# Kernel optimization log

Hardware: AMD Instinct MI355X
Metric: run time of the kernel (lower is better)

## Reference

```python
import jax, jax.numpy as jnp
import numpy as np

B, L, DM, DI, N = 8, 2048, 512, 768, 8  # batch, seq, d_model, d_inner=int(1.5*512), d_state


def setup_inputs() -> dict:
    key = jax.random.key(0)
    ks = jax.random.split(key, 8)
    g = lambda k, shape, sc=1.0: (jax.random.normal(k, shape, jnp.float32) * sc)
    return {
        "x": g(ks[0], (B, L, DM)),
        "W_in": g(ks[1], (DM, 2 * DI), 0.02),    # in_proj weight (stored in->out)
        "A_log": g(ks[2], (DI, N)),               # nn.Parameter(randn)
        "D_param": g(ks[3], (DI,)),               # skip-connection D
        "W_x": g(ks[4], (DI, N), 0.02),           # x_proj weight
        "W_dt": g(ks[5], (N, DI), 0.02),          # dt_proj weight
        "b_dt": jnp.zeros((DI,), jnp.float32),    # dt_proj bias
        "W_out": g(ks[6], (DI, DM), 0.02),        # out_proj weight
    }


def reference(x, W_in, A_log, D_param, W_x, W_dt, b_dt, W_out):
    xz = x @ W_in                                  # (B,L,2*DI)
    d_inner = W_in.shape[1] // 2
    x_ssm, z = xz[..., :d_inner], xz[..., d_inner:]
    x_ssm = jax.nn.silu(x_ssm)                     # (B,L,DI)
    A = -jnp.exp(A_log.astype(jnp.float32))        # (DI,N)
    delta = jax.nn.softplus((x_ssm @ W_x) @ W_dt + b_dt)  # (B,L,DI)

    n_state = A.shape[-1]

    def step(h, inp):
        xt, dt = inp                               # each (B,DI)
        dA = jnp.exp(dt[..., None] * A)            # (B,DI,N)
        h = dA * h + dt[..., None] * xt[..., None]
        y = jnp.sum(h, axis=-1) + D_param * xt     # (B,DI)
        return h, y

    h0 = jnp.zeros((x.shape[0], d_inner, n_state), x_ssm.dtype)
    xs = (jnp.swapaxes(x_ssm, 0, 1), jnp.swapaxes(delta, 0, 1))  # (L,B,DI)
    _, ys = jax.lax.scan(step, h0, xs)             # ys: (L,B,DI)
    y = jnp.swapaxes(ys, 0, 1)                     # (B,L,DI)
    y = y * jax.nn.silu(z)
    return y @ W_out                               # (B,L,DM)
```

## Files before the change

### kernel.cpp

```cpp
#include <hip/hip_runtime.h>

typedef unsigned short bfu;
typedef __attribute__((ext_vector_type(8))) short short8;
typedef __attribute__((ext_vector_type(4))) float f32x4;

__device__ __forceinline__ float bf2f(bfu u){
  union { unsigned int i; float f; } v; v.i = ((unsigned int)u) << 16; return v.f;
}
__device__ __forceinline__ bfu f2bf(float f){
  union { float f; unsigned int i; } v; v.f = f;
  unsigned int r = (v.i + 0x7FFFu + ((v.i >> 16) & 1u)) >> 16;
  return (bfu)r;
}
__device__ __forceinline__ float fexp2(float x){ return __builtin_amdgcn_exp2f(x); }
__device__ __forceinline__ float flog2(float x){ return __builtin_amdgcn_logf(x); }
__device__ __forceinline__ float softplusf(float x){
  float t = fexp2(-fabsf(x) * 1.44269504088896f);
  return fmaxf(x, 0.f) + 0.69314718055995f * flog2(1.f + t);
}
__device__ __forceinline__ void gload16(const bfu* g, bfu* l){
  __builtin_amdgcn_global_load_lds((const __attribute__((address_space(1))) unsigned int*)g,
                                   (__attribute__((address_space(3))) unsigned int*)l, 16, 0, 0);
}

__global__ __launch_bounds__(256) void cvt_all_kernel(const float* __restrict__ x, bfu* __restrict__ x_bf,
                                                      const float* __restrict__ W_in, const float* __restrict__ W_out,
                                                      const float* __restrict__ W_x,
                                                      bfu* __restrict__ WinT, bfu* __restrict__ WoutT,
                                                      float* __restrict__ WxT){
  int g = blockIdx.x * 256 + threadIdx.x;
  if (g < 2097152){
    float4 v = ((const float4*)x)[g];
    ushort4 o;
    o.x = f2bf(v.x); o.y = f2bf(v.y); o.z = f2bf(v.z); o.w = f2bf(v.w);
    ((ushort4*)x_bf)[g] = o;
    return;
  }
  int h = g - 2097152;
  if (h < 786432){
    int r = h % 512, c = h / 512;
    WinT[h] = f2bf(W_in[(size_t)r * 1536 + c]);
  } else if (h < 786432 + 393216){
    int h2 = h - 786432;
    int r = h2 % 768, c = h2 / 768;
    WoutT[h2] = f2bf(W_out[(size_t)r * 512 + c]);
  } else if (h < 786432 + 393216 + 6144){
    int h2 = h - (786432 + 393216);
    int n = h2 / 768, k = h2 % 768;
    WxT[h2] = W_x[(size_t)k * 8 + n];
  }
}

template<int EPI, int KK>
__global__ __launch_bounds__(256)
void gemm_db(const bfu* __restrict__ Amat, const bfu* __restrict__ Bt,
             void* __restrict__ out0, void* __restrict__ out1,
             int NBN, int N)
{
  constexpr int NT = KK / 64;
  __shared__ bfu As[2 * 128 * 64];
  __shared__ bfu Bs[2 * 128 * 64];
  const int tid  = threadIdx.x;
  const int lane = tid & 63;
  const int w    = tid >> 6;
  const int wr   = w >> 1, wc = w & 1;

  const int cpx = gridDim.x >> 3;
  const int id  = blockIdx.x;
  const int nid = (id & 7) * cpx + (id >> 3);
  const int bn  = nid % NBN;
  const int bm  = nid / NBN;

  const int srow = tid >> 3;
  const int scol = ((tid & 7) ^ (srow & 7)) * 8;
  const bfu* gA = Amat + ((size_t)(bm * 128 + srow)) * KK + scol;
  const bfu* gB = Bt   + ((size_t)(bn * 128 + srow)) * KK + scol;
  bfu* lA = As + tid * 8;
  bfu* lB = Bs + tid * 8;

  auto STAGE = [&](int t, int sel){
    const int k0 = t * 64;
    #pragma unroll
    for (int i = 0; i < 4; i++){
      gload16(gA + (size_t)(i * 32) * KK + k0, lA + sel * 8192 + i * 2048);
      gload16(gB + (size_t)(i * 32) * KK + k0, lB + sel * 8192 + i * 2048);
    }
  };

  f32x4 acc[4][4];
  #pragma unroll
  for (int i = 0; i < 4; i++)
    #pragma unroll
    for (int j = 0; j < 4; j++)
      #pragma unroll
      for (int r = 0; r < 4; r++) acc[i][j][r] = 0.f;

  STAGE(0, 0);
  STAGE(1, 1);

  #pragma unroll
  for (int t = 0; t < NT; ++t){
    if (t + 1 < NT) asm volatile("s_waitcnt vmcnt(8)" ::: "memory");
    else            asm volatile("s_waitcnt vmcnt(0)" ::: "memory");
    __builtin_amdgcn_s_barrier();

    const bfu* Ab = As + (t & 1) * 8192;
    const bfu* Bb = Bs + (t & 1) * 8192;
    #pragma unroll
    for (int kk = 0; kk < 2; kk++){
      short8 a[4], b[4];
      const int sA = ((kk * 4 + (lane >> 4)) ^ (lane & 7)) * 8;
      #pragma unroll
      for (int m = 0; m < 4; m++){
        int r = wr * 64 + m * 16 + (lane & 15);
        a[m] = *(const short8*)&Ab[r * 64 + sA];
      }
      #pragma unroll
      for (int n = 0; n < 4; n++){
        int r = wc * 64 + n * 16 + (lane & 15);
        b[n] = *(const short8*)&Bb[r * 64 + sA];
      }
      __builtin_amdgcn_s_setprio(1);
      #pragma unroll
      for (int m = 0; m < 4; m++)
        #pragma unroll
        for (int n = 0; n < 4; n++)
          acc[m][n] = __builtin_amdgcn_mfma_f32_16x16x32_bf16(a[m], b[n], acc[m][n], 0, 0, 0);
      __builtin_amdgcn_s_setprio(0);
    }
    __builtin_amdgcn_s_barrier();
    if (t + 2 < NT) STAGE(t + 2, t & 1);
  }

  #pragma unroll
  for (int m = 0; m < 4; m++){
    #pragma unroll
    for (int n = 0; n < 4; n++){
      const int row0 = bm * 128 + wr * 64 + m * 16 + (lane >> 4) * 4;
      const int col  = bn * 128 + wc * 64 + n * 16 + (lane & 15);
      #pragma unroll
      for (int r = 0; r < 4; r++){
        float v = acc[m][n][r];
        int row = row0 + r;
        if (EPI == 0){
          float s = v / (1.f + __expf(-v));
          if (col < 768) ((bfu*)out0)[(size_t)row * 768 + col]         = f2bf(s);
          else           ((bfu*)out1)[(size_t)row * 768 + (col - 768)] = f2bf(s);
        } else {
          ((float*)out0)[(size_t)row * N + col] = v;
        }
      }
    }
  }
}

__global__ __launch_bounds__(256) void u_kernel(const bfu* __restrict__ xssm, const float* __restrict__ WxT,
                                                float* __restrict__ u){
  int wid = threadIdx.x >> 6, lane = threadIdx.x & 63;
  int row = blockIdx.x * 4 + wid;
  const bfu* xr = xssm + (size_t)row * 768;
  float acc[8];
  #pragma unroll
  for (int n = 0; n < 8; n++) acc[n] = 0.f;
  #pragma unroll
  for (int i = 0; i < 3; i++){
    int kb = i * 256 + lane * 4;
    ushort4 xq = *(const ushort4*)(xr + kb);
    float x0 = bf2f(xq.x), x1 = bf2f(xq.y), x2 = bf2f(xq.z), x3 = bf2f(xq.w);
    #pragma unroll
    for (int n = 0; n < 8; n++){
      float4 wv = *(const float4*)(WxT + (size_t)n * 768 + kb);
      acc[n] += x0 * wv.x + x1 * wv.y + x2 * wv.z + x3 * wv.w;
    }
  }
  #pragma unroll
  for (int n = 0; n < 8; n++){
    #pragma unroll
    for (int off = 32; off >= 1; off >>= 1) acc[n] += __shfl_xor(acc[n], off, 64);
  }
  if (lane == 0){
    float4 o0 = { acc[0], acc[1], acc[2], acc[3] };
    float4 o1 = { acc[4], acc[5], acc[6], acc[7] };
    *(float4*)(u + (size_t)row * 8)     = o0;
    *(float4*)(u + (size_t)row * 8 + 4) = o1;
  }
}

__global__ __launch_bounds__(128) void scan_phase1(const bfu* __restrict__ xssm, const float* __restrict__ u,
    const float* __restrict__ Wdt, const float* __restrict__ bdt, const float* __restrict__ A_log,
    float* __restrict__ Pws, float* __restrict__ Hws){
  int tid = threadIdx.x;
  int bid = blockIdx.x;
  int b = bid / 192; int rem = bid % 192;
  int c = rem / 3;   int dblk = rem % 3;
  int d0 = dblk * 256 + tid * 2;
  float Al2[2][8], H[2][8], Wr[2][8], bd[2], S[2];
  #pragma unroll
  for (int j = 0; j < 2; j++){
    bd[j] = bdt[d0 + j];
    S[j] = 0.f;
    #pragma unroll
    for (int n = 0; n < 8; n++){
      Al2[j][n] = -__expf(A_log[(size_t)(d0 + j) * 8 + n]) * 1.4426950408889634f;
      Wr[j][n]  = Wdt[(size_t)n * 768 + d0 + j];
      H[j][n] = 0.f;
    }
  }
  int r0 = b * 2048 + c * 32;
  size_t base = (size_t)r0 * 768 + d0;
  #pragma unroll 8
  for (int i = 0; i < 32; i++){
    float4 u0 = *(const float4*)(u + (size_t)(r0 + i) * 8);
    float4 u1 = *(const float4*)(u + (size_t)(r0 + i) * 8 + 4);
    ushort2 xq = *(const ushort2*)(xssm + base + (size_t)i * 768);
    #pragma unroll
    for (int j = 0; j < 2; j++){
      float xt = bf2f(j == 0 ? xq.x : xq.y);
      float dv = bd[j] + u0.x * Wr[j][0] + u0.y * Wr[j][1] + u0.z * Wr[j][2] + u0.w * Wr[j][3]
                       + u1.x * Wr[j][4] + u1.y * Wr[j][5] + u1.z * Wr[j][6] + u1.w * Wr[j][7];
      float dt = softplusf(dv);
      float dx = dt * xt;
      S[j] += dt;
      #pragma unroll
      for (int n = 0; n < 8; n++){
        float e = fexp2(dt * Al2[j][n]);
        H[j][n] = e * H[j][n] + dx;
      }
    }
  }
  size_t o = (((size_t)b * 64 + c) * 768 + d0) * 8;
  #pragma unroll
  for (int j = 0; j < 2; j++){
    float4 p0, p1;
    p0.x = fexp2(S[j] * Al2[j][0]); p0.y = fexp2(S[j] * Al2[j][1]);
    p0.z = fexp2(S[j] * Al2[j][2]); p0.w = fexp2(S[j] * Al2[j][3]);
    p1.x = fexp2(S[j] * Al2[j][4]); p1.y = fexp2(S[j] * Al2[j][5]);
    p1.z = fexp2(S[j] * Al2[j][6]); p1.w = fexp2(S[j] * Al2[j][7]);
    float4 h0 = { H[j][0], H[j][1], H[j][2], H[j][3] };
    float4 h1 = { H[j][4], H[j][5], H[j][6], H[j][7] };
    *(float4*)(Pws + o + j * 8)     = p0;
    *(float4*)(Pws + o + j * 8 + 4) = p1;
    *(float4*)(Hws + o + j * 8)     = h0;
    *(float4*)(Hws + o + j * 8 + 4) = h1;
  }
}

__global__ __launch_bounds__(256) void scan_phase2(float* __restrict__ Pws, const float* __restrict__ Hws){
  int g = blockIdx.x * 256 + threadIdx.x;
  int within = g % 6144;
  int b = g / 6144;
  size_t base = (size_t)b * 64 * 6144 + within;
  float hin = 0.f;
  #pragma unroll 8
  for (int c = 0; c < 64; c++){
    size_t idx = base + (size_t)c * 6144;
    float p = Pws[idx], hh = Hws[idx];
    Pws[idx] = hin;
    hin = p * hin + hh;
  }
}

__global__ __launch_bounds__(128) void scan_phase3(const bfu* __restrict__ xssm, const float* __restrict__ u,
    const float* __restrict__ Wdt, const float* __restrict__ bdt, const float* __restrict__ A_log,
    const float* __restrict__ Dp, const bfu* __restrict__ siluz, const float* __restrict__ Hin,
    bfu* __restrict__ yz){
  int tid = threadIdx.x;
  int bid = blockIdx.x;
  int b = bid / 192; int rem = bid % 192;
  int c = rem / 3;   int dblk = rem % 3;
  int d0 = dblk * 256 + tid * 2;
  float Al2[2][8], H[2][8], Wr[2][8], bd[2], Dd[2];
  size_t o = (((size_t)b * 64 + c) * 768 + d0) * 8;
  #pragma unroll
  for (int j = 0; j < 2; j++){
    bd[j] = bdt[d0 + j];
    Dd[j] = Dp[d0 + j];
    float4 h0 = *(const float4*)(Hin + o + j * 8);
    float4 h1 = *(const float4*)(Hin + o + j * 8 + 4);
    H[j][0] = h0.x; H[j][1] = h0.y; H[j][2] = h0.z; H[j][3] = h0.w;
    H[j][4] = h1.x; H[j][5] = h1.y; H[j][6] = h1.z; H[j][7] = h1.w;
    #pragma unroll
    for (int n = 0; n < 8; n++){
      Al2[j][n] = -__expf(A_log[(size_t)(d0 + j) * 8 + n]) * 1.4426950408889634f;
      Wr[j][n]  = Wdt[(size_t)n * 768 + d0 + j];
    }
  }
  int r0 = b * 2048 + c * 32;
  size_t base = (size_t)r0 * 768 + d0;
  #pragma unroll 8
  for (int i = 0; i < 32; i++){
    float4 u0 = *(const float4*)(u + (size_t)(r0 + i) * 8);
    float4 u1 = *(const float4*)(u + (size_t)(r0 + i) * 8 + 4);
    ushort2 xq = *(const ushort2*)(xssm + base + (size_t)i * 768);
    ushort2 zq = *(const ushort2*)(siluz + base + (size_t)i * 768);
    ushort2 oq;
    #pragma unroll
    for (int j = 0; j < 2; j++){
      float xt = bf2f(j == 0 ? xq.x : xq.y);
      float dv = bd[j] + u0.x * Wr[j][0] + u0.y * Wr[j][1] + u0.z * Wr[j][2] + u0.w * Wr[j][3]
                       + u1.x * Wr[j][4] + u1.y * Wr[j][5] + u1.z * Wr[j][6] + u1.w * Wr[j][7];
      float dt = softplusf(dv);
      float dx = dt * xt;
      float y = Dd[j] * xt;
      #pragma unroll
      for (int n = 0; n < 8; n++){
        float e = fexp2(dt * Al2[j][n]);
        H[j][n] = e * H[j][n] + dx;
        y += H[j][n];
      }
      float sz = bf2f(j == 0 ? zq.x : zq.y);
      bfu r = f2bf(y * sz);
      if (j == 0) oq.x = r; else oq.y = r;
    }
    *(ushort2*)(yz + base + (size_t)i * 768) = oq;
  }
}

extern "C" void kernel_launch(void* const* d_in, const int* in_sizes, int n_in,
                              void* d_out, int out_size, void* d_ws, size_t ws_size,
                              hipStream_t stream){
  const float* x     = (const float*)d_in[0];
  const float* W_in  = (const float*)d_in[1];
  const float* A_log = (const float*)d_in[2];
  const float* D_par = (const float*)d_in[3];
  const float* W_x   = (const float*)d_in[4];
  const float* W_dt  = (const float*)d_in[5];
  const float* b_dt  = (const float*)d_in[6];
  const float* W_out = (const float*)d_in[7];
  float* out = (float*)d_out;
  (void)in_sizes; (void)n_in; (void)out_size; (void)ws_size;

  char* base = (char*)d_ws;
  size_t off = 0;
  auto alloc = [&](size_t bytes)->char*{
    char* p = base + off; off += (bytes + 255) & ~(size_t)255; return p;
  };
  bfu*   x_bf  = (bfu*)  alloc((size_t)16384 * 512 * 2);
  bfu*   WinT  = (bfu*)  alloc((size_t)1536 * 512 * 2);
  bfu*   WoutT = (bfu*)  alloc((size_t)512 * 768 * 2);
  float* WxT   = (float*)alloc((size_t)8 * 768 * 4);
  bfu*   xssm  = (bfu*)  alloc((size_t)16384 * 768 * 2);
  bfu*   siluz = (bfu*)  alloc((size_t)16384 * 768 * 2);
  float* u     = (float*)alloc((size_t)16384 * 8 * 4);
  float* Pws   = (float*)alloc((size_t)8 * 64 * 768 * 8 * 4);
  float* Hws   = (float*)alloc((size_t)8 * 64 * 768 * 8 * 4);
  bfu*   yz    = (bfu*)  alloc((size_t)16384 * 768 * 2);

  cvt_all_kernel<<<12824, 256, 0, stream>>>(x, x_bf, W_in, W_out, W_x, WinT, WoutT, WxT);
  gemm_db<0, 512><<<1536, 256, 0, stream>>>(x_bf, WinT, xssm, siluz, 12, 1536);
  u_kernel<<<4096, 256, 0, stream>>>(xssm, WxT, u);
  scan_phase1<<<1536, 128, 0, stream>>>(xssm, u, W_dt, b_dt, A_log, Pws, Hws);
  scan_phase2<<<192, 256, 0, stream>>>(Pws, Hws);
  scan_phase3<<<1536, 128, 0, stream>>>(xssm, u, W_dt, b_dt, A_log, D_par, siluz, Pws, yz);
  gemm_db<1, 768><<<512, 256, 0, stream>>>(yz, WoutT, out, nullptr, 4, 512);
}
```

Baseline: 168.5 us.

## Replace double-buffered GEMM with single-buffered variant and taller tiles for in_proj

The GEMM kernel drops its two-stage LDS double buffering and async prefetch, and the setprio hints around the MFMA block. Each k-step now loads, syncs, computes and syncs again. The tile height becomes a template parameter, and in_proj switches to 256x128 tiles with 512 threads at half the grid size. This halves LDS per tile and simplifies the loop. The cost is that global-to-LDS loads no longer overlap with MFMA compute.

```diff
diff --git a/kernel.cpp b/kernel.cpp
--- a/kernel.cpp
+++ b/kernel.cpp
@@ -51,15 +51,17 @@
   }
 }
 
-template<int EPI, int KK>
-__global__ __launch_bounds__(256)
-void gemm_db(const bfu* __restrict__ Amat, const bfu* __restrict__ Bt,
+template<int EPI, int BM, int KK>
+__global__ __launch_bounds__(BM * 2)
+void gemm_sb(const bfu* __restrict__ Amat, const bfu* __restrict__ Bt,
              void* __restrict__ out0, void* __restrict__ out1,
              int NBN, int N)
 {
-  constexpr int NT = KK / 64;
-  __shared__ bfu As[2 * 128 * 64];
-  __shared__ bfu Bs[2 * 128 * 64];
+  constexpr int BN = 128;
+  constexpr int THREADS = BM * 2;
+  constexpr int RPI = THREADS / 8;
+  __shared__ bfu As[BM * 64];
+  __shared__ bfu Bs[BN * 64];
   const int tid  = threadIdx.x;
   const int lane = tid & 63;
   const int w    = tid >> 6;
@@ -73,19 +75,10 @@
 
   const int srow = tid >> 3;
   const int scol = ((tid & 7) ^ (srow & 7)) * 8;
-  const bfu* gA = Amat + ((size_t)(bm * 128 + srow)) * KK + scol;
-  const bfu* gB = Bt   + ((size_t)(bn * 128 + srow)) * KK + scol;
-  bfu* lA = As + tid * 8;
-  bfu* lB = Bs + tid * 8;
-
-  auto STAGE = [&](int t, int sel){
-    const int k0 = t * 64;
-    #pragma unroll
-    for (int i = 0; i < 4; i++){
-      gload16(gA + (size_t)(i * 32) * KK + k0, lA + sel * 8192 + i * 2048);
-      gload16(gB + (size_t)(i * 32) * KK + k0, lB + sel * 8192 + i * 2048);
-    }
-  };
+  const bfu* gA = Amat + ((size_t)(bm * BM + srow)) * KK + scol;
+  const bfu* gB = Bt   + ((size_t)(bn * BN + srow)) * KK + scol;
+  bfu* lA = As + srow * 64 + (tid & 7) * 8;
+  bfu* lB = Bs + srow * 64 + (tid & 7) * 8;
 
   f32x4 acc[4][4];
   #pragma unroll
@@ -95,17 +88,15 @@
       #pragma unroll
       for (int r = 0; r < 4; r++) acc[i][j][r] = 0.f;
 
-  STAGE(0, 0);
-  STAGE(1, 1);
-
-  #pragma unroll
-  for (int t = 0; t < NT; ++t){
-    if (t + 1 < NT) asm volatile("s_waitcnt vmcnt(8)" ::: "memory");
-    else            asm volatile("s_waitcnt vmcnt(0)" ::: "memory");
-    __builtin_amdgcn_s_barrier();
-
-    const bfu* Ab = As + (t & 1) * 8192;
-    const bfu* Bb = Bs + (t & 1) * 8192;
+  for (int k0 = 0; k0 < KK; k0 += 64){
+    #pragma unroll
+    for (int i = 0; i < BM / RPI; i++)
+      gload16(gA + (size_t)(i * RPI) * KK + k0, lA + i * RPI * 64);
+    #pragma unroll
+    for (int j = 0; j < BN / RPI; j++)
+      gload16(gB + (size_t)(j * RPI) * KK + k0, lB + j * RPI * 64);
+    __syncthreads();
+
     #pragma unroll
     for (int kk = 0; kk < 2; kk++){
       short8 a[4], b[4];
@@ -113,31 +104,28 @@
       #pragma unroll
       for (int m = 0; m < 4; m++){
         int r = wr * 64 + m * 16 + (lane & 15);
-        a[m] = *(const short8*)&Ab[r * 64 + sA];
+        a[m] = *(const short8*)&As[r * 64 + sA];
       }
       #pragma unroll
       for (int n = 0; n < 4; n++){
         int r = wc * 64 + n * 16 + (lane & 15);
-        b[n] = *(const short8*)&Bb[r * 64 + sA];
-      }
-      __builtin_amdgcn_s_setprio(1);
+        b[n] = *(const short8*)&Bs[r * 64 + sA];
+      }
       #pragma unroll
       for (int m = 0; m < 4; m++)
         #pragma unroll
         for (int n = 0; n < 4; n++)
           acc[m][n] = __builtin_amdgcn_mfma_f32_16x16x32_bf16(a[m], b[n], acc[m][n], 0, 0, 0);
-      __builtin_amdgcn_s_setprio(0);
-    }
-    __builtin_amdgcn_s_barrier();
-    if (t + 2 < NT) STAGE(t + 2, t & 1);
+    }
+    __syncthreads();
   }
 
   #pragma unroll
   for (int m = 0; m < 4; m++){
     #pragma unroll
     for (int n = 0; n < 4; n++){
-      const int row0 = bm * 128 + wr * 64 + m * 16 + (lane >> 4) * 4;
-      const int col  = bn * 128 + wc * 64 + n * 16 + (lane & 15);
+      const int row0 = bm * BM + wr * 64 + m * 16 + (lane >> 4) * 4;
+      const int col  = bn * BN + wc * 64 + n * 16 + (lane & 15);
       #pragma unroll
       for (int r = 0; r < 4; r++){
         float v = acc[m][n][r];
@@ -347,10 +335,10 @@
   bfu*   yz    = (bfu*)  alloc((size_t)16384 * 768 * 2);
 
   cvt_all_kernel<<<12824, 256, 0, stream>>>(x, x_bf, W_in, W_out, W_x, WinT, WoutT, WxT);
-  gemm_db<0, 512><<<1536, 256, 0, stream>>>(x_bf, WinT, xssm, siluz, 12, 1536);
+  gemm_sb<0, 256, 512><<<768, 512, 0, stream>>>(x_bf, WinT, xssm, siluz, 12, 1536);
   u_kernel<<<4096, 256, 0, stream>>>(xssm, WxT, u);
   scan_phase1<<<1536, 128, 0, stream>>>(xssm, u, W_dt, b_dt, A_log, Pws, Hws);
   scan_phase2<<<192, 256, 0, stream>>>(Pws, Hws);
   scan_phase3<<<1536, 128, 0, stream>>>(xssm, u, W_dt, b_dt, A_log, D_par, siluz, Pws, yz);
-  gemm_db<1, 768><<<512, 256, 0, stream>>>(yz, WoutT, out, nullptr, 4, 512);
-}
+  gemm_sb<1, 128, 768><<<512, 256, 0, stream>>>(yz, WoutT, out, nullptr, 4, 512);
+}
```

Result: faster. 163.2 us (-3.1%).
